# Kernel optimization log

Hardware: AMD Instinct MI355X
Metric: run time of the kernel (lower is better)

The kernel has to match this reference:

```python
import jax, jax.numpy as jnp
import numpy as np

B, S, D, H = 4, 2048, 1024, 16
HD = D // H
THETA = 10000.0


def rope(x, pos, theta=THETA):
    # x: [..., seq, d], pos: broadcastable to [..., seq]
    d = x.shape[-1]
    half = d // 2
    inv_freq = 1.0 / (theta ** (jnp.arange(half, dtype=jnp.float32) * 2.0 / d))  # [half]
    ang = pos[..., None].astype(jnp.float32) * inv_freq  # [..., seq, half]
    cos, sin = jnp.cos(ang), jnp.sin(ang)
    x1, x2 = x[..., 0::2], x[..., 1::2]
    r1 = x1 * cos - x2 * sin
    r2 = x1 * sin + x2 * cos
    return jnp.stack([r1, r2], axis=-1).reshape(x.shape).astype(x.dtype)


def setup_inputs() -> dict:
    key = jax.random.key(0)
    ks = jax.random.split(key, 5)
    x = jax.random.normal(ks[0], (B, S, D), dtype=jnp.float32)
    token_positions = jnp.tile(jnp.arange(S, dtype=jnp.int64 if jax.config.jax_enable_x64 else jnp.int32), (B, 1))
    scale = 0.02
    Wq = jax.random.normal(ks[1], (D, D), dtype=jnp.float32) * scale
    Wk = jax.random.normal(ks[2], (D, D), dtype=jnp.float32) * scale
    Wv = jax.random.normal(ks[3], (D, D), dtype=jnp.float32) * scale
    Wo = jax.random.normal(ks[4], (D, D), dtype=jnp.float32) * scale
    return {"x": x, "token_positions": token_positions, "Wq": Wq, "Wk": Wk, "Wv": Wv, "Wo": Wo}


def reference(x, token_positions, Wq, Wk, Wv, Wo):
    b, s, d = x.shape
    # QKV projections (torch Linear: x @ W.T), split heads -> [b, h, s, hd]
    def proj(W):
        y = jnp.einsum('bsd,ed->bse', x, W)
        return y.reshape(b, s, H, HD).transpose(0, 2, 1, 3)
    Q, K, V = proj(Wq), proj(Wk), proj(Wv)
    # token_positions [..., seq] -> [..., 1, seq] to broadcast over heads
    pos = token_positions[:, None, :]  # [b, 1, s]
    Q = rope(Q, pos)
    K = rope(K, pos)
    # causal mask and scaled dot-product attention
    idx = jnp.arange(s)
    causal = idx[:, None] >= idx[None, :]  # [s, s], query >= key
    scores = jnp.einsum('bhqd,bhkd->bhqk', Q, K) / jnp.sqrt(jnp.float32(HD))
    scores = jnp.where(causal, scores, -jnp.inf)
    weights = jax.nn.softmax(scores, axis=-1)
    o = jnp.einsum('bhqk,bhkd->bhqd', weights, V)
    o = o.transpose(0, 2, 1, 3).reshape(b, s, d)  # merge heads
    return jnp.einsum('bsd,ed->bse', o, Wo)
```

## Files before the change

### kernel.cpp

```cpp
#include <hip/hip_runtime.h>

#define S_LEN 2048
#define NH 16
#define HDIM 64
#define DMODEL 1024

typedef __attribute__((ext_vector_type(8))) short bf16x8;
typedef __attribute__((ext_vector_type(4))) float f32x4;

__device__ __forceinline__ short f2bf(float f) {
    union { float f; unsigned u; } x; x.f = f;
    unsigned r = x.u + 0x7fffu + ((x.u >> 16) & 1u);
    return (short)(r >> 16);
}

#define GLDS(g, l) __builtin_amdgcn_global_load_lds( \
    (__attribute__((address_space(1))) void*)(g),    \
    (__attribute__((address_space(3))) void*)(l), 16, 0, 0)

#define QSCALE 0.18033688011112042f
#define FREQ_L 0.41524101186109327f

__global__ __launch_bounds__(256) void prep(const float* __restrict__ x,
                                            const float* __restrict__ wq,
                                            const float* __restrict__ wk,
                                            const float* __restrict__ wv,
                                            const float* __restrict__ wo,
                                            const int* __restrict__ tp,
                                            short* __restrict__ xb,
                                            short* __restrict__ wqb,
                                            short* __restrict__ wkb,
                                            short* __restrict__ wvb,
                                            short* __restrict__ wob,
                                            float2* __restrict__ tab) {
    int bid = blockIdx.x;
    if (bid < 8192) {
        int i = bid * 256 + threadIdx.x;
        float4 v = ((const float4*)x)[i];
        short4 o;
        o.x = f2bf(v.x); o.y = f2bf(v.y); o.z = f2bf(v.z); o.w = f2bf(v.w);
        ((short4*)xb)[i] = o;
    } else if (bid < 12288) {
        int sel = (bid - 8192) >> 10;
        const float* in = sel == 0 ? wq : sel == 1 ? wk : sel == 2 ? wv : wo;
        short* out = sel == 0 ? wqb : sel == 1 ? wkb : sel == 2 ? wvb : wob;
        int i = ((bid - 8192) & 1023) * 256 + threadIdx.x;
        float4 v = ((const float4*)in)[i];
        short4 o;
        o.x = f2bf(v.x); o.y = f2bf(v.y); o.z = f2bf(v.z); o.w = f2bf(v.w);
        ((short4*)out)[i] = o;
    } else {
        int idx = (bid - 12288) * 256 + threadIdx.x;
        int b = idx >> 16, s = (idx >> 5) & 2047, i = idx & 31;
        float p = (float)tp[(b << 11) + s];
        float freq = exp2f(-(float)i * FREQ_L);
        float sn, cs;
        sincosf(p * freq, &sn, &cs);
        tab[idx] = make_float2(cs, sn);
    }
}

__global__ __launch_bounds__(512) void gemm_qkv(const short* __restrict__ A,
                                                const short* __restrict__ Bq,
                                                const short* __restrict__ Bk,
                                                const short* __restrict__ Bv,
                                                const float2* __restrict__ tab,
                                                short* __restrict__ Qo,
                                                short* __restrict__ Ko,
                                                short* __restrict__ Vo) {
    constexpr int K = 1024;
    __shared__ __align__(16) short smem[4 * 12288];

    const int sel = blockIdx.x >> 3;
    const int bn = blockIdx.x & 7;
    const int bm = blockIdx.y;
    const short* Bm = sel == 0 ? Bq : sel == 1 ? Bk : Bv;
    short* Cb = sel == 0 ? Qo : sel == 1 ? Ko : Vo;

    const int tid = threadIdx.x;
    const int lane = tid & 63;
    const int w = tid >> 6;
    const int wm = w >> 1;
    const int wn = w & 1;
    const int quad = lane >> 4, l16 = lane & 15;

    int aoff[2], boffv;
#pragma unroll
    for (int i = 0; i < 2; i++) {
        int Lc = i * 512 + tid;
        int row = Lc >> 2;
        int gc = (Lc & 3) ^ ((row >> 1) & 3);
        aoff[i] = (bm * 256 + row) * K + gc * 8;
    }
    {
        int row = tid >> 2;
        int gc = (tid & 3) ^ ((row >> 1) & 3);
        boffv = (bn * 128 + row) * K + gc * 8;
    }

    auto stage = [&](int h) {
        char* slotB = (char*)smem + (h & 3) * 24576;
        const int kh = h * 32;
#pragma unroll
        for (int i = 0; i < 2; i++)
            GLDS(A + aoff[i] + kh, slotB + i * 8192 + w * 1024);
        GLDS(Bm + boffv + kh, slotB + 16384 + w * 1024);
    };

    f32x4 acc[4][4] = {};
    const int rsw = (quad ^ ((l16 >> 1) & 3)) * 8;

    auto compute = [&](int h) {
        const short* sA = smem + (h & 3) * 12288;
        const short* sB = sA + 8192;
        bf16x8 af[4], bfm[4];
#pragma unroll
        for (int mi = 0; mi < 4; mi++)
            af[mi] = *(const bf16x8*)&sA[(wm * 64 + mi * 16 + l16) * 32 + rsw];
#pragma unroll
        for (int ni = 0; ni < 4; ni++)
            bfm[ni] = *(const bf16x8*)&sB[(wn * 64 + ni * 16 + l16) * 32 + rsw];
        __builtin_amdgcn_s_setprio(1);
#pragma unroll
        for (int mi = 0; mi < 4; mi++)
#pragma unroll
            for (int ni = 0; ni < 4; ni++)
                acc[mi][ni] = __builtin_amdgcn_mfma_f32_16x16x32_bf16(af[mi], bfm[ni],
                                                                      acc[mi][ni], 0, 0, 0);
        __builtin_amdgcn_s_setprio(0);
    };

    stage(0); stage(1); stage(2);

    for (int h = 0; h < 29; ++h) {
        asm volatile("s_waitcnt vmcnt(6)" ::: "memory");
        __builtin_amdgcn_s_barrier();
        __builtin_amdgcn_sched_barrier(0);
        stage(h + 3);
        compute(h);
    }
    asm volatile("s_waitcnt vmcnt(6)" ::: "memory");
    __builtin_amdgcn_s_barrier();
    __builtin_amdgcn_sched_barrier(0);
    compute(29);
    asm volatile("s_waitcnt vmcnt(3)" ::: "memory");
    __builtin_amdgcn_s_barrier();
    __builtin_amdgcn_sched_barrier(0);
    compute(30);
    asm volatile("s_waitcnt vmcnt(0)" ::: "memory");
    __builtin_amdgcn_s_barrier();
    __builtin_amdgcn_sched_barrier(0);
    compute(31);

    const int gm0 = bm * 256 + wm * 64;
    const int gn0 = bn * 128 + wn * 64;

    if (sel == 2) {
        short* T = smem;
        __syncthreads();
#pragma unroll
        for (int mi = 0; mi < 4; mi++) {
            int lmb = wm * 64 + mi * 16 + quad * 4;
#pragma unroll
            for (int ni = 0; ni < 4; ni++) {
                int ln = wn * 64 + ni * 16 + l16;
                short4 pk;
                pk.x = f2bf(acc[mi][ni][0]);
                pk.y = f2bf(acc[mi][ni][1]);
                pk.z = f2bf(acc[mi][ni][2]);
                pk.w = f2bf(acc[mi][ni][3]);
                *(short4*)&T[ln * 256 + (lmb ^ ((ln & 31) << 3))] = pk;
            }
        }
        __syncthreads();
        const int row = tid >> 2, qt = tid & 3;
        const int grow = bn * 128 + row;
        const int gb = bm >> 3;
        const int gs0 = (bm & 7) * 256;
        short* dst = Cb + (((size_t)(gb * NH + (grow >> 6)) * HDIM + (grow & 63)) * S_LEN
                           + gs0 + qt * 64);
#pragma unroll
        for (int j = 0; j < 8; j++) {
            bf16x8 v = *(const bf16x8*)&T[row * 256 +
                        ((qt * 64 + j * 8) ^ ((row & 31) << 3))];
            *(bf16x8*)(dst + j * 8) = v;
        }
    } else {
        const float qs = (sel == 0) ? QSCALE : 1.0f;
#pragma unroll
        for (int mi = 0; mi < 4; mi++)
#pragma unroll
            for (int r = 0; r < 4; r++) {
                int gm = gm0 + mi * 16 + quad * 4 + r;
                const float2* trow = tab + (gm << 5);
                int b = gm >> 11, s = gm & 2047;
#pragma unroll
                for (int ni = 0; ni < 4; ni++) {
                    float2 cs = trow[ni * 8 + (l16 >> 1)];
                    float v = acc[mi][ni][r];
                    float prt = __shfl_xor(v, 1, 64);
                    float val = (l16 & 1) ? (prt * cs.y + v * cs.x)
                                          : (v * cs.x - prt * cs.y);
                    int gn = gn0 + ni * 16 + l16;
                    int h = gn >> 6, hd = gn & 63;
                    Cb[((b * NH + h) * S_LEN + s) * HDIM + hd] = f2bf(val * qs);
                }
            }
    }
}

__global__ __launch_bounds__(256) void gemm_o(const short* __restrict__ A,
                                              const short* __restrict__ Bw,
                                              float* __restrict__ Cf) {
    constexpr int N = 1024, K = 1024, BK = 32;
    __shared__ __align__(16) short sa[3][128 * BK];
    __shared__ __align__(16) short sb[3][64 * BK];

    const int tid = threadIdx.x;
    const int lane = tid & 63;
    const int w = tid >> 6;
    const int quad = lane >> 4, l16 = lane & 15;
    const int bn = blockIdx.x, bm = blockIdx.y;
    const int arow0 = bm * 128, brow0 = bn * 64;

    int aoff[2], boff;
#pragma unroll
    for (int i = 0; i < 2; i++) {
        int cs = i * 256 + tid;
        int row = cs >> 2;
        int gc = (cs & 3) ^ ((row >> 1) & 3);
        aoff[i] = (arow0 + row) * K + gc * 8;
    }
    {
        int row = tid >> 2;
        int gc = (tid & 3) ^ ((row >> 1) & 3);
        boff = (brow0 + row) * K + gc * 8;
    }

    auto stage = [&](int kt, int b) {
        const int k0 = kt * BK;
#pragma unroll
        for (int i = 0; i < 2; i++)
            GLDS(A + aoff[i] + k0, (char*)&sa[b][0] + i * 4096 + w * 1024);
        GLDS(Bw + boff + k0, (char*)&sb[b][0] + w * 1024);
    };

    f32x4 acc[2][4] = {};
    const int rsw = (quad ^ ((l16 >> 1) & 3)) * 8;

    auto compute = [&](int b) {
        bf16x8 af[2];
#pragma unroll
        for (int mi = 0; mi < 2; mi++)
            af[mi] = *(const bf16x8*)&sa[b][(w * 32 + mi * 16 + l16) * BK + rsw];
#pragma unroll
        for (int ni = 0; ni < 4; ni++) {
            bf16x8 bfr = *(const bf16x8*)&sb[b][(ni * 16 + l16) * BK + rsw];
#pragma unroll
            for (int mi = 0; mi < 2; mi++)
                acc[mi][ni] = __builtin_amdgcn_mfma_f32_16x16x32_bf16(af[mi], bfr,
                                                                     acc[mi][ni], 0, 0, 0);
        }
    };

    stage(0, 0);
    stage(1, 1);

    auto step = [&](int kt, int b, int bs) {
        asm volatile("s_waitcnt vmcnt(3)" ::: "memory");
        __builtin_amdgcn_s_barrier();
        __builtin_amdgcn_sched_barrier(0);
        stage(kt + 2, bs);
        compute(b);
    };

    for (int kt = 0; kt < 30; kt += 3) {
        step(kt + 0, 0, 2);
        step(kt + 1, 1, 0);
        step(kt + 2, 2, 1);
    }
    asm volatile("s_waitcnt vmcnt(3)" ::: "memory");
    __builtin_amdgcn_s_barrier();
    __builtin_amdgcn_sched_barrier(0);
    compute(0);
    asm volatile("s_waitcnt vmcnt(0)" ::: "memory");
    __builtin_amdgcn_s_barrier();
    __builtin_amdgcn_sched_barrier(0);
    compute(1);

    const int gm0 = arow0 + w * 32;
#pragma unroll
    for (int mi = 0; mi < 2; mi++)
#pragma unroll
        for (int ni = 0; ni < 4; ni++)
#pragma unroll
            for (int r = 0; r < 4; r++) {
                int gm = gm0 + mi * 16 + quad * 4 + r;
                int gn = brow0 + ni * 16 + l16;
                Cf[gm * N + gn] = acc[mi][ni][r];
            }
}

__global__ __launch_bounds__(256, 3) void attn(const short* __restrict__ Q,
                                               const short* __restrict__ Km,
                                               const short* __restrict__ Vt,
                                               short* __restrict__ O) {
    __shared__ __align__(16) short kbuf[2][64 * 64];
    __shared__ __align__(16) short vbuf[2][64 * 64];
    __shared__ __align__(16) short pbuf[4][32 * 64];

    const int lane = threadIdx.x & 63;
    const int w = threadIdx.x >> 6;
    const int quad = lane >> 4, l16 = lane & 15;
    const int l7 = l16 & 7;
    const int bh = blockIdx.y;

    const short* Qg = Q  + bh * S_LEN * 64;
    const short* Kg = Km + bh * S_LEN * 64;
    const short* Vg = Vt + bh * 64 * S_LEN;
    short* myp = &pbuf[w][0];

    const int b = bh >> 4, h = bh & 15;

    bf16x8 ones;
#pragma unroll
    for (int j = 0; j < 8; j++) ones[j] = (short)0x3f80;

    auto stage = [&](int kt, int par) {
        const short* kt_base = Kg + kt * 64 * 64;
        const short* vt_base = Vg + kt * 64;
#pragma unroll
        for (int i = 0; i < 2; ++i) {
            int ch = w * 128 + i * 64 + lane;
            int row = ch >> 3;
            int c = (ch & 7) ^ (row & 7);
            GLDS(kt_base + row * 64 + c * 8, (char*)&kbuf[par][(w * 128 + i * 64) * 8]);
        }
#pragma unroll
        for (int i = 0; i < 2; ++i) {
            int ch = w * 128 + i * 64 + lane;
            int row = ch >> 3;
            int c = (ch & 7) ^ (row & 7);
            GLDS(vt_base + row * S_LEN + c * 8, (char*)&vbuf[par][(w * 128 + i * 64) * 8]);
        }
    };

    const int QtA = blockIdx.x;
    const int QtB = 15 - blockIdx.x;

    stage(0, 0);
    int t = 0;

    for (int phase = 0; phase < 2; ++phase) {
        const int Qt = phase ? QtB : QtA;
        const int nkt = 2 * Qt + 2;

        bf16x8 aq[2][2];
#pragma unroll
        for (int mi = 0; mi < 2; mi++) {
            int qrow = Qt * 128 + w * 32 + mi * 16 + l16;
#pragma unroll
            for (int kc = 0; kc < 2; kc++)
                aq[mi][kc] = *(const bf16x8*)&Qg[qrow * 64 + kc * 32 + quad * 8];
        }

        f32x4 oacc[2][4] = {};
        f32x4 lacc[2] = {};

        for (int kt = 0; kt < nkt; ++kt, ++t) {
            __syncthreads();
            if (kt + 1 < nkt)    stage(kt + 1, (t + 1) & 1);
            else if (phase == 0) stage(0,      (t + 1) & 1);
            const short* kb_cur = &kbuf[t & 1][0];
            const short* vb_cur = &vbuf[t & 1][0];

            f32x4 sc[2][4] = {};
#pragma unroll
            for (int nt = 0; nt < 4; nt++) {
                int raddr = (nt * 16 + l16) * 64;
#pragma unroll
                for (int kc = 0; kc < 2; kc++) {
                    bf16x8 kf = *(const bf16x8*)&kb_cur[raddr + (((quad + kc * 4) ^ l7) * 8)];
                    sc[0][nt] = __builtin_amdgcn_mfma_f32_16x16x32_bf16(aq[0][kc], kf, sc[0][nt], 0, 0, 0);
                    sc[1][nt] = __builtin_amdgcn_mfma_f32_16x16x32_bf16(aq[1][kc], kf, sc[1][nt], 0, 0, 0);
                }
            }
            if (kt >= nkt - 2) {
#pragma unroll
                for (int mi = 0; mi < 2; mi++)
#pragma unroll
                    for (int nt = 0; nt < 4; nt++)
#pragma unroll
                        for (int r = 0; r < 4; r++) {
                            int col = kt * 64 + nt * 16 + l16;
                            int row = Qt * 128 + w * 32 + mi * 16 + quad * 4 + r;
                            if (col > row) sc[mi][nt][r] = -__builtin_inff();
                        }
            }
#pragma unroll
            for (int mi = 0; mi < 2; mi++)
#pragma unroll
                for (int nt = 0; nt < 4; nt++)
#pragma unroll
                    for (int r = 0; r < 4; r++) {
                        float pv = __builtin_amdgcn_exp2f(sc[mi][nt][r]);
                        int q = mi * 16 + quad * 4 + r;
                        union { float f; unsigned short us[2]; } uu;
                        uu.f = pv;
                        myp[q * 64 + (((nt * 2 + (l16 >> 3)) ^ (q & 7)) * 8) + l7] =
                            (short)uu.us[1];
                    }
            bf16x8 ap[2][2];
#pragma unroll
            for (int mi = 0; mi < 2; mi++)
#pragma unroll
                for (int kc = 0; kc < 2; kc++)
                    ap[mi][kc] = *(const bf16x8*)&myp[(mi * 16 + l16) * 64 +
                                                      (((quad + kc * 4) ^ l7) * 8)];
#pragma unroll
            for (int nt = 0; nt < 4; nt++) {
                int raddr = (nt * 16 + l16) * 64;
#pragma unroll
                for (int kc = 0; kc < 2; kc++) {
                    bf16x8 vf = *(const bf16x8*)&vb_cur[raddr + (((quad + kc * 4) ^ l7) * 8)];
                    oacc[0][nt] = __builtin_amdgcn_mfma_f32_16x16x32_bf16(ap[0][kc], vf, oacc[0][nt], 0, 0, 0);
                    oacc[1][nt] = __builtin_amdgcn_mfma_f32_16x16x32_bf16(ap[1][kc], vf, oacc[1][nt], 0, 0, 0);
                }
            }
#pragma unroll
            for (int mi = 0; mi < 2; mi++) {
                lacc[mi] = __builtin_amdgcn_mfma_f32_16x16x32_bf16(ap[mi][0], ones, lacc[mi], 0, 0, 0);
                lacc[mi] = __builtin_amdgcn_mfma_f32_16x16x32_bf16(ap[mi][1], ones, lacc[mi], 0, 0, 0);
            }
        }
#pragma unroll
        for (int mi = 0; mi < 2; mi++)
#pragma unroll
            for (int r = 0; r < 4; r++) {
                float inv = 1.0f / lacc[mi][r];
                int srow = Qt * 128 + w * 32 + mi * 16 + quad * 4 + r;
#pragma unroll
                for (int nt = 0; nt < 4; nt++) {
                    int hd = nt * 16 + l16;
                    O[(b * S_LEN + srow) * DMODEL + h * HDIM + hd] = f2bf(oacc[mi][nt][r] * inv);
                }
            }
    }
}

extern "C" void kernel_launch(void* const* d_in, const int* in_sizes, int n_in,
                              void* d_out, int out_size, void* d_ws, size_t ws_size,
                              hipStream_t stream) {
    const float* x  = (const float*)d_in[0];
    const int*   tp = (const int*)d_in[1];
    const float* Wq = (const float*)d_in[2];
    const float* Wk = (const float*)d_in[3];
    const float* Wv = (const float*)d_in[4];
    const float* Wo = (const float*)d_in[5];
    float* out = (float*)d_out;

    char* ws = (char*)d_ws;
    const size_t MB = 1024 * 1024;
    short* xb  = (short*)(ws);
    short* wqb = (short*)(ws + 16 * MB);
    short* wkb = (short*)(ws + 18 * MB);
    short* wvb = (short*)(ws + 20 * MB);
    short* wob = (short*)(ws + 22 * MB);
    short* Qb  = (short*)(ws + 24 * MB);
    short* Kb  = (short*)(ws + 40 * MB);
    short* Vtb = (short*)(ws + 56 * MB);
    float2* tab = (float2*)d_out;

    prep<<<13312, 256, 0, stream>>>(x, Wq, Wk, Wv, Wo, tp,
                                    xb, wqb, wkb, wvb, wob, tab);

    gemm_qkv<<<dim3(24, 32), 512, 0, stream>>>(xb, wqb, wkb, wvb, tab, Qb, Kb, Vtb);

    attn<<<dim3(8, 64), 256, 0, stream>>>(Qb, Kb, Vtb, xb);

    gemm_o<<<dim3(16, 64), 256, 0, stream>>>(xb, wob, out);
}
```

Before: 254.4 us.

## Deepen QKV GEMM k-tile to 64 with triple-buffered LDS pipeline

The QKV projection GEMM now stages 64-wide k-slices instead of 32, using three LDS buffers in place of four. The swizzle changes to an 8-chunk XOR pattern, and the main loop is unrolled by three to rotate the buffer slots. This halves the number of barrier/waitcnt iterations and gives more MFMA work between syncs. In exchange it raises LDS use to 144KB per block, which may limit occupancy, and the pipeline is one stage shallower.

Measured after the change: 258.8 us. Within noise of the previous version (+1.7%).

```diff
diff --git a/kernel.cpp b/kernel.cpp
--- a/kernel.cpp
+++ b/kernel.cpp
@@ -69,7 +69,7 @@
                                                 short* __restrict__ Ko,
                                                 short* __restrict__ Vo) {
     constexpr int K = 1024;
-    __shared__ __align__(16) short smem[4 * 12288];
+    __shared__ __align__(16) short smem[3 * 24576];
 
     const int sel = blockIdx.x >> 3;
     const int bn = blockIdx.x & 7;
@@ -83,74 +83,86 @@
     const int wm = w >> 1;
     const int wn = w & 1;
     const int quad = lane >> 4, l16 = lane & 15;
-
-    int aoff[2], boffv;
+    const int l7 = l16 & 7;
+
+    int aoff[4], boff[2];
+#pragma unroll
+    for (int i = 0; i < 4; i++) {
+        int Lc = i * 512 + tid;
+        int row = Lc >> 3;
+        int cc = (Lc & 7) ^ (row & 7);
+        aoff[i] = (bm * 256 + row) * K + cc * 8;
+    }
 #pragma unroll
     for (int i = 0; i < 2; i++) {
         int Lc = i * 512 + tid;
-        int row = Lc >> 2;
-        int gc = (Lc & 3) ^ ((row >> 1) & 3);
-        aoff[i] = (bm * 256 + row) * K + gc * 8;
-    }
-    {
-        int row = tid >> 2;
-        int gc = (tid & 3) ^ ((row >> 1) & 3);
-        boffv = (bn * 128 + row) * K + gc * 8;
-    }
-
-    auto stage = [&](int h) {
-        char* slotB = (char*)smem + (h & 3) * 24576;
-        const int kh = h * 32;
+        int row = Lc >> 3;
+        int cc = (Lc & 7) ^ (row & 7);
+        boff[i] = (bn * 128 + row) * K + cc * 8;
+    }
+
+    auto stage = [&](int h, int slot) {
+        char* sbase = (char*)smem + slot * 49152;
+        const int kh = h * 64;
+#pragma unroll
+        for (int i = 0; i < 4; i++)
+            GLDS(A + aoff[i] + kh, sbase + i * 8192 + w * 1024);
 #pragma unroll
         for (int i = 0; i < 2; i++)
-            GLDS(A + aoff[i] + kh, slotB + i * 8192 + w * 1024);
-        GLDS(Bm + boffv + kh, slotB + 16384 + w * 1024);
+            GLDS(Bm + boff[i] + kh, sbase + 32768 + i * 8192 + w * 1024);
     };
 
     f32x4 acc[4][4] = {};
-    const int rsw = (quad ^ ((l16 >> 1) & 3)) * 8;
-
-    auto compute = [&](int h) {
-        const short* sA = smem + (h & 3) * 12288;
-        const short* sB = sA + 8192;
-        bf16x8 af[4], bfm[4];
-#pragma unroll
-        for (int mi = 0; mi < 4; mi++)
-            af[mi] = *(const bf16x8*)&sA[(wm * 64 + mi * 16 + l16) * 32 + rsw];
-#pragma unroll
-        for (int ni = 0; ni < 4; ni++)
-            bfm[ni] = *(const bf16x8*)&sB[(wn * 64 + ni * 16 + l16) * 32 + rsw];
-        __builtin_amdgcn_s_setprio(1);
-#pragma unroll
-        for (int mi = 0; mi < 4; mi++)
+
+    auto compute = [&](int slot) {
+        const short* sA = smem + slot * 24576;
+        const short* sB = sA + 16384;
+#pragma unroll
+        for (int kc = 0; kc < 2; kc++) {
+            const int c = ((kc * 4 + quad) ^ l7) * 8;
+            bf16x8 af[4], bfm[4];
+#pragma unroll
+            for (int mi = 0; mi < 4; mi++)
+                af[mi] = *(const bf16x8*)&sA[(wm * 64 + mi * 16 + l16) * 64 + c];
 #pragma unroll
             for (int ni = 0; ni < 4; ni++)
-                acc[mi][ni] = __builtin_amdgcn_mfma_f32_16x16x32_bf16(af[mi], bfm[ni],
-                                                                      acc[mi][ni], 0, 0, 0);
-        __builtin_amdgcn_s_setprio(0);
-    };
-
-    stage(0); stage(1); stage(2);
-
-    for (int h = 0; h < 29; ++h) {
+                bfm[ni] = *(const bf16x8*)&sB[(wn * 64 + ni * 16 + l16) * 64 + c];
+            __builtin_amdgcn_s_setprio(1);
+#pragma unroll
+            for (int mi = 0; mi < 4; mi++)
+#pragma unroll
+                for (int ni = 0; ni < 4; ni++)
+                    acc[mi][ni] = __builtin_amdgcn_mfma_f32_16x16x32_bf16(af[mi], bfm[ni],
+                                                                          acc[mi][ni], 0, 0, 0);
+            __builtin_amdgcn_s_setprio(0);
+        }
+    };
+
+    stage(0, 0); stage(1, 1);
+
+    auto step = [&](int h, int sc, int ss) {
         asm volatile("s_waitcnt vmcnt(6)" ::: "memory");
         __builtin_amdgcn_s_barrier();
         __builtin_amdgcn_sched_barrier(0);
-        stage(h + 3);
-        compute(h);
-    }
+        stage(h + 2, ss);
+        compute(sc);
+    };
+
+    for (int h = 0; h < 12; h += 3) {
+        step(h + 0, 0, 2);
+        step(h + 1, 1, 0);
+        step(h + 2, 2, 1);
+    }
+    step(12, 0, 2);
+    step(13, 1, 0);
     asm volatile("s_waitcnt vmcnt(6)" ::: "memory");
     __builtin_amdgcn_s_barrier();
     __builtin_amdgcn_sched_barrier(0);
-    compute(29);
-    asm volatile("s_waitcnt vmcnt(3)" ::: "memory");
-    __builtin_amdgcn_s_barrier();
-    __builtin_amdgcn_sched_barrier(0);
-    compute(30);
+    compute(2);
     asm volatile("s_waitcnt vmcnt(0)" ::: "memory");
     __builtin_amdgcn_s_barrier();
     __builtin_amdgcn_sched_barrier(0);
-    compute(31);
+    compute(0);
 
     const int gm0 = bm * 256 + wm * 64;
     const int gn0 = bn * 128 + wn * 64;
```
